# Kernel optimization log

Measured on AMD Instinct MI355X. Metric: run time of the kernel, lower is better.

The kernel has to match this reference:

```python
import jax, jax.numpy as jnp
import numpy as np

# Static config (matches init_kwargs)
B, S = 4, 1024            # prefill: 4 sequences of 1024 tokens (num_tokens = 4096)
H = 16                    # num_heads
NOPE, ROPE, VD = 128, 64, 128
RANK = 512                # kv_lora_rank
SCALE = 0.07216878364870323  # 1/sqrt(head_dim=192)


def setup_inputs() -> dict:
    key = jax.random.key(0)
    k1, k2, k3, k4 = jax.random.split(key, 4)
    T = B * S
    return {
        "q": jax.random.normal(k1, (T, H, NOPE + ROPE), dtype=jnp.float32),
        "compressed_kv": jax.random.normal(k2, (T, RANK), dtype=jnp.float32),
        "rope_k": jax.random.normal(k3, (T, ROPE), dtype=jnp.float32),
        "w_up": jax.random.normal(k4, (H * (NOPE + VD), RANK), dtype=jnp.float32) * 0.02,
    }


def reference(q, compressed_kv, rope_k, w_up):
    T = q.shape[0]
    # Up-project latent -> per-head (k_nope, v): [T, H, NOPE+VD]
    kv = (compressed_kv @ w_up.T).reshape(B, S, H, NOPE + VD)
    k_nope = kv[..., :NOPE]          # [B,S,H,NOPE]
    v = kv[..., NOPE:]               # [B,S,H,VD]

    qb = q.reshape(B, S, H, NOPE + ROPE)
    q_nope = qb[..., :NOPE]          # [B,S,H,NOPE]
    q_rope = qb[..., NOPE:]          # [B,S,H,ROPE]
    rk = rope_k.reshape(B, S, ROPE)  # head-shared RoPE K component

    # Attention logits: nope part (per-head K) + rope part (shared K)
    scores = jnp.einsum('bqhd,bkhd->bhqk', q_nope, k_nope)
    scores = scores + jnp.einsum('bqhd,bkd->bhqk', q_rope, rk)
    scores = scores * SCALE

    # Causal mask within each sequence
    causal = jnp.tril(jnp.ones((S, S), dtype=bool))
    scores = jnp.where(causal[None, None], scores, jnp.finfo(scores.dtype).min)

    p = jax.nn.softmax(scores, axis=-1)                 # [B,H,S,S]
    out = jnp.einsum('bhqk,bkhd->bqhd', p, v)           # [B,S,H,VD]
    return out.reshape(T, H, VD)
```

## Files before the change

### kernel.cpp

```cpp
#include <hip/hip_runtime.h>
#include <stdint.h>


#define Hz 16
#define Sz 1024
#define RANKz 512
#define SCALEf 0.07216878364870323f
#define CRr(r) ((((r) & 3)) + 8 * ((r) >> 2) + 4 * hi)

typedef unsigned short u16;
typedef __attribute__((ext_vector_type(8))) short bf16x8;
typedef __attribute__((ext_vector_type(4))) float f32x4;
typedef __attribute__((ext_vector_type(16))) float f32x16;

__device__ __forceinline__ u16 f2b(float f) {
  union { float f; uint32_t u; } x; x.f = f;
  return (u16)((x.u + 0x7fffu + ((x.u >> 16) & 1u)) >> 16);
}
__device__ __forceinline__ uint32_t cvtpk(float lo, float hi_) {
  uint32_t r;
  asm("v_cvt_pk_bf16_f32 %0, %1, %2" : "=v"(r) : "v"(lo), "v"(hi_));
  return r;
}

__global__ void cvt_bf16_kernel(const float* __restrict__ a, u16* __restrict__ ao,
                                const float* __restrict__ b, u16* __restrict__ bo,
                                const float* __restrict__ c, u16* __restrict__ co,
                                int na, int nb) {
  int idx = blockIdx.x * blockDim.x + threadIdx.x;
  const float* s; u16* d; int i;
  if (idx < na)            { s = a; d = ao; i = idx; }
  else if (idx < na + nb)  { s = b; d = bo; i = idx - na; }
  else                     { s = c; d = co; i = idx - na - nb; }
  float4 v = ((const float4*)s)[i];
  ushort4 o = make_ushort4(f2b(v.x), f2b(v.y), f2b(v.z), f2b(v.w));
  ((ushort4*)d)[i] = o;
}

__global__ __launch_bounds__(256)
void gemm_kv_bf16(const u16* __restrict__ A,
                  const u16* __restrict__ Bm,
                  u16* __restrict__ C) {
  __shared__ u16 As[128 * 32];
  __shared__ u16 Bs[128 * 32];
  const int tid = threadIdx.x;
  const int w = tid >> 6, lane = tid & 63;
  const int wr = w >> 1, wc = w & 1;
  const int row0 = blockIdx.x * 128, col0 = blockIdx.y * 128;
  f32x4 acc[4][4];
#pragma unroll
  for (int m = 0; m < 4; ++m)
#pragma unroll
    for (int n = 0; n < 4; ++n) acc[m][n] = (f32x4){0.f, 0.f, 0.f, 0.f};

  const int rstage = (lane >> 2);
  const int cstage = (lane & 3) * 8;

  for (int kt = 0; kt < RANKz / 32; ++kt) {
    const int k0 = kt * 32;
#pragma unroll
    for (int i = 0; i < 2; ++i) {
      const int chunk = i * 4 + w;
      const int r = chunk * 16 + rstage;
      const u16* ga = A  + (size_t)(row0 + r) * RANKz + k0 + cstage;
      const u16* gb = Bm + (size_t)(col0 + r) * RANKz + k0 + cstage;
      __builtin_amdgcn_global_load_lds((const __attribute__((address_space(1))) void*)ga,
                                       (__attribute__((address_space(3))) void*)&As[chunk * 512], 16, 0, 0);
      __builtin_amdgcn_global_load_lds((const __attribute__((address_space(1))) void*)gb,
                                       (__attribute__((address_space(3))) void*)&Bs[chunk * 512], 16, 0, 0);
    }
    __syncthreads();
    const int klo = (lane >> 4) * 8;
    bf16x8 af[4], bfr[4];
#pragma unroll
    for (int m = 0; m < 4; ++m)
      af[m] = *(const bf16x8*)&As[(wr * 64 + m * 16 + (lane & 15)) * 32 + klo];
#pragma unroll
    for (int n = 0; n < 4; ++n)
      bfr[n] = *(const bf16x8*)&Bs[(wc * 64 + n * 16 + (lane & 15)) * 32 + klo];
#pragma unroll
    for (int m = 0; m < 4; ++m)
#pragma unroll
      for (int n = 0; n < 4; ++n)
        acc[m][n] = __builtin_amdgcn_mfma_f32_16x16x32_bf16(af[m], bfr[n], acc[m][n], 0, 0, 0);
    __syncthreads();
  }
  const int cb = col0 + wc * 64 + (lane & 15);
  const int rb = row0 + wr * 64 + (lane >> 4) * 4;
#pragma unroll
  for (int m = 0; m < 4; ++m)
#pragma unroll
    for (int n = 0; n < 4; ++n)
#pragma unroll
      for (int j = 0; j < 4; ++j)
        C[(size_t)(rb + m * 16 + j) * 4096 + (cb + n * 16)] = f2b(acc[m][n][j]);
}

__global__ __launch_bounds__(512, 2)
void mla_attn_mfma(const float* __restrict__ q,
                   const u16* __restrict__ kvb,
                   const u16* __restrict__ ropeb,
                   float* __restrict__ out) {
  __shared__ __align__(16) unsigned char LB[81920];

  const int tid = threadIdx.x;
  const int w = tid >> 6, lane = tid & 63;
  const int l31 = lane & 31, hi = lane >> 5;
  const int half = w >> 2, strip = w & 3;

  const int bid = blockIdx.x;
  const int hb = bid >> 6;
  const int qt = (hb < 4) ? (7 - hb) : (hb - 4);
  const int bh = (bid & 7) * 8 + ((bid >> 3) & 7);
  const int bat = bh >> 4, h = bh & 15;
  const int tok0 = bat * Sz;
  const int q0 = qt * 128 + strip * 32;
  const int ntiles = 2 * qt + 2;

  const int vkp = tid & 31, vdc = tid >> 5;
  uint4 va, vb;

  auto stageK = [&](int tokt, int buf) {
#pragma unroll
    for (int i = 0; i < 2; ++i) {
      const int c = w * 2 + i;
      const int row = c * 4 + (lane >> 4);
      const int sc = (lane & 15) ^ (row & 7);
      const u16* src = kvb + ((size_t)(tokt + row) * Hz + h) * 256 + sc * 8;
      __builtin_amdgcn_global_load_lds((const __attribute__((address_space(1))) void*)src,
                                       (__attribute__((address_space(3))) void*)(LB + buf * 16384 + c * 1024), 16, 0, 0);
    }
    {
      const int c = w;
      const int row = c * 8 + (lane >> 3);
      const int sc = (lane & 7) ^ (row & 7);
      const u16* src = ropeb + (size_t)(tokt + row) * 64 + sc * 8;
      __builtin_amdgcn_global_load_lds((const __attribute__((address_space(1))) void*)src,
                                       (__attribute__((address_space(3))) void*)(LB + 32768 + buf * 8192 + c * 1024), 16, 0, 0);
    }
  };
  auto loadV = [&](int tokt) {
    const u16* vp = kvb + ((size_t)(tokt + vkp * 2) * Hz + h) * 256 + 128 + vdc * 8;
    va = *(const uint4*)vp;
    vb = *(const uint4*)(vp + Hz * 256);
  };
  auto writeVt = [&](int buf) {
    union { uint4 v; u16 u[8]; } A_, B_;
    A_.v = va; B_.v = vb;
    uint32_t* vt = (uint32_t*)(LB + 49152 + buf * 16384);
#pragma unroll
    for (int i = 0; i < 8; ++i) {
      const int d = vdc * 8 + i;
      vt[d * 32 + 4 * ((vkp >> 2) ^ (d & 7)) + (vkp & 3)] =
          (uint32_t)A_.u[i] | ((uint32_t)B_.u[i] << 16);
    }
  };

  bf16x8 qf[12];
  {
    const float* qp = q + ((size_t)(tok0 + q0 + l31) * Hz + h) * 192 + hi * 8;
#pragma unroll
    for (int ds = 0; ds < 12; ++ds) {
      float4 a = *(const float4*)(qp + ds * 16);
      float4 b = *(const float4*)(qp + ds * 16 + 4);
      union { bf16x8 v; u16 u[8]; } t;
      t.u[0] = f2b(a.x * SCALEf); t.u[1] = f2b(a.y * SCALEf);
      t.u[2] = f2b(a.z * SCALEf); t.u[3] = f2b(a.w * SCALEf);
      t.u[4] = f2b(b.x * SCALEf); t.u[5] = f2b(b.y * SCALEf);
      t.u[6] = f2b(b.z * SCALEf); t.u[7] = f2b(b.w * SCALEf);
      qf[ds] = t.v;
    }
  }

  f32x16 acc[4];
#pragma unroll
  for (int db = 0; db < 4; ++db)
#pragma unroll
    for (int r = 0; r < 16; ++r) acc[db][r] = 0.f;
  float m_run = -1e30f, l_run = 0.f;

  stageK(tok0, 0);
  loadV(tok0);
  __syncthreads();
  writeVt(0);
  __syncthreads();

#pragma unroll 1
  for (int t = 0; t < ntiles; ++t) {
    const int cur = t & 1;
    const bool havenext = (t + 1 < ntiles);
    if (havenext) {
      stageK(tok0 + (t + 1) * 64, cur ^ 1);
      loadV(tok0 + (t + 1) * 64);
    }

    const int kb = t * 64 + half * 32;
    if (kb <= q0 + 31) {
      const u16* KnC = (const u16*)(LB + cur * 16384);
      const u16* KrC = (const u16*)(LB + 32768 + cur * 8192);
      const int row_a = half * 32 + l31;
      const int swz = row_a & 7;

      f32x16 s0;
#pragma unroll
      for (int r = 0; r < 16; ++r) s0[r] = 0.f;
      __builtin_amdgcn_s_setprio(1);
#pragma unroll
      for (int ds = 0; ds < 8; ++ds) {
        bf16x8 kf = *(const bf16x8*)&KnC[row_a * 128 + 8 * ((2 * ds + hi) ^ swz)];
        s0 = __builtin_amdgcn_mfma_f32_32x32x16_bf16(kf, qf[ds], s0, 0, 0, 0);
      }
#pragma unroll
      for (int ds = 8; ds < 12; ++ds) {
        bf16x8 kf = *(const bf16x8*)&KrC[row_a * 64 + 8 * ((2 * (ds - 8) + hi) ^ swz)];
        s0 = __builtin_amdgcn_mfma_f32_32x32x16_bf16(kf, qf[ds], s0, 0, 0, 0);
      }
      __builtin_amdgcn_s_setprio(0);

      if (kb + 31 > q0) {
#pragma unroll
        for (int r = 0; r < 16; ++r)
          if (kb + CRr(r) > q0 + l31) s0[r] = -1e30f;
      }

      float mx = s0[0];
#pragma unroll
      for (int r = 1; r < 16; ++r) mx = fmaxf(mx, s0[r]);
      mx = fmaxf(mx, __shfl_xor(mx, 32));
      if (__any(mx > m_run + 8.f)) {
        const float nm = fmaxf(m_run, mx);
        const float cr = __expf(m_run - nm);
        m_run = nm; l_run *= cr;
#pragma unroll
        for (int r = 0; r < 16; ++r) {
          const float crg = __shfl(cr, CRr(r));
#pragma unroll
          for (int db = 0; db < 4; ++db) acc[db][r] *= crg;
        }
      }
      float ts = 0.f;
#pragma unroll
      for (int r = 0; r < 16; ++r) { s0[r] = __expf(s0[r] - m_run); ts += s0[r]; }
      ts += __shfl_xor(ts, 32);
      l_run += ts;

      bf16x8 pf[2];
#pragma unroll
      for (int ks = 0; ks < 2; ++ks) {
        const int o = ks * 8;
        const uint32_t w0 = cvtpk(s0[o + 0], s0[o + 1]);
        const uint32_t w1 = cvtpk(s0[o + 4], s0[o + 5]);
        const uint32_t w2 = cvtpk(s0[o + 2], s0[o + 3]);
        const uint32_t w3 = cvtpk(s0[o + 6], s0[o + 7]);
        const uint32_t t0 = __shfl_xor(w0, 32), t1 = __shfl_xor(w1, 32);
        const uint32_t t2 = __shfl_xor(w2, 32), t3 = __shfl_xor(w3, 32);
        union { bf16x8 v; uint32_t u[4]; } P;
        P.u[0] = hi ? t1 : w0;
        P.u[1] = hi ? t3 : w2;
        P.u[2] = hi ? w1 : t0;
        P.u[3] = hi ? w3 : t2;
        pf[ks] = P.v;
      }

      const u16* VtC = (const u16*)(LB + 49152 + cur * 16384);
      __builtin_amdgcn_s_setprio(1);
#pragma unroll
      for (int ks = 0; ks < 2; ++ks)
#pragma unroll
        for (int db = 0; db < 4; ++db) {
          const int d = db * 32 + l31;
          bf16x8 vf = *(const bf16x8*)&VtC[d * 64 + 8 * ((half * 4 + 2 * ks + hi) ^ (d & 7))];
          acc[db] = __builtin_amdgcn_mfma_f32_32x32x16_bf16(pf[ks], vf, acc[db], 0, 0, 0);
        }
      __builtin_amdgcn_s_setprio(0);
    }

    if (havenext) writeVt(cur ^ 1);
    __syncthreads();
  }

  float* mb = (float*)LB;
  float* ml = (float*)(LB + 65536);
  if (half == 1) {
#pragma unroll
    for (int db = 0; db < 4; ++db)
#pragma unroll
      for (int g = 0; g < 4; ++g) {
        float4 v = make_float4(acc[db][g * 4 + 0], acc[db][g * 4 + 1],
                               acc[db][g * 4 + 2], acc[db][g * 4 + 3]);
        *(float4*)&mb[strip * 4096 + db * 1024 + g * 256 + lane * 4] = v;
      }
    if (lane < 32) { ml[strip * 64 + lane] = m_run; ml[strip * 64 + 32 + lane] = l_run; }
  }
  __syncthreads();
  if (half == 0) {
    const float mp = ml[strip * 64 + l31];
    const float lp = ml[strip * 64 + 32 + l31];
    const float M  = fmaxf(m_run, mp);
    const float sA = __expf(m_run - M);
    const float sB = __expf(mp - M);
    const float inv = 1.0f / (l_run * sA + lp * sB);
    const float fAl = sA * inv, fBl = sB * inv;
    float fA[16], fB[16];
#pragma unroll
    for (int r = 0; r < 16; ++r) { fA[r] = __shfl(fAl, CRr(r)); fB[r] = __shfl(fBl, CRr(r)); }
#pragma unroll
    for (int db = 0; db < 4; ++db)
#pragma unroll
      for (int g = 0; g < 4; ++g) {
        float4 pv = *(const float4*)&mb[strip * 4096 + db * 1024 + g * 256 + lane * 4];
#pragma unroll
        for (int jj = 0; jj < 4; ++jj) {
          const int r = g * 4 + jj;
          const float pvj = (jj == 0) ? pv.x : (jj == 1) ? pv.y : (jj == 2) ? pv.z : pv.w;
          out[((size_t)(tok0 + q0 + CRr(r)) * Hz + h) * 128 + db * 32 + l31] =
              acc[db][r] * fA[r] + pvj * fB[r];
        }
      }
  }
}

extern "C" void kernel_launch(void* const* d_in, const int* in_sizes, int n_in,
                              void* d_out, int out_size, void* d_ws, size_t ws_size,
                              hipStream_t stream) {
  const float* q    = (const float*)d_in[0];
  const float* ckv  = (const float*)d_in[1];
  const float* rope = (const float*)d_in[2];
  const float* wup  = (const float*)d_in[3];
  float* out = (float*)d_out;

  u16* ckvb  = (u16*)d_ws;
  u16* wupb  = ckvb + (size_t)4096 * RANKz;
  u16* kvb   = wupb + (size_t)4096 * RANKz;
  u16* ropeb = kvb + (size_t)4096 * 4096;

  const int nvec = 4096 * RANKz / 4;
  const int nrope = 4096 * 64 / 4;
  cvt_bf16_kernel<<<(2 * nvec + nrope) / 256, 256, 0, stream>>>(ckv, ckvb, wup, wupb, rope, ropeb, nvec, nvec);

  dim3 gg(32, 32);
  gemm_kv_bf16<<<gg, 256, 0, stream>>>(ckvb, wupb, kvb);

  mla_attn_mfma<<<512, 512, 0, stream>>>(q, kvb, ropeb, out);
}
```

Measured before the change: 105.3 us.

## Pair causal q-tiles per block and triple-buffer K/V with distance-2 prefetch

Each block now processes two query tiles (qt and 7-qt) in sequence, so every block does the same amount of causal work. The grid halves to 256 blocks at one block per CU. K, rope-K and V tiles are triple-buffered with prefetch two tiles ahead, using explicit vmcnt waits and raw barriers in place of __syncthreads. LDS grows to about 121KB and occupancy drops to one block per CU, which risks less latency hiding between blocks. The max and sum reductions are also rewritten as trees.

```diff
diff --git a/kernel.cpp b/kernel.cpp
--- a/kernel.cpp
+++ b/kernel.cpp
@@ -96,12 +96,12 @@
         C[(size_t)(rb + m * 16 + j) * 4096 + (cb + n * 16)] = f2b(acc[m][n][j]);
 }
 
-__global__ __launch_bounds__(512, 2)
+__global__ __launch_bounds__(512, 1)
 void mla_attn_mfma(const float* __restrict__ q,
                    const u16* __restrict__ kvb,
                    const u16* __restrict__ ropeb,
                    float* __restrict__ out) {
-  __shared__ __align__(16) unsigned char LB[81920];
+  __shared__ __align__(16) unsigned char LB[123904];
 
   const int tid = threadIdx.x;
   const int w = tid >> 6, lane = tid & 63;
@@ -109,16 +109,12 @@
   const int half = w >> 2, strip = w & 3;
 
   const int bid = blockIdx.x;
-  const int hb = bid >> 6;
-  const int qt = (hb < 4) ? (7 - hb) : (hb - 4);
-  const int bh = (bid & 7) * 8 + ((bid >> 3) & 7);
+  const int job = (bid & 7) * 32 + (bid >> 3);
+  const int bh = job >> 2, pr = job & 3;
   const int bat = bh >> 4, h = bh & 15;
   const int tok0 = bat * Sz;
-  const int q0 = qt * 128 + strip * 32;
-  const int ntiles = 2 * qt + 2;
 
   const int vkp = tid & 31, vdc = tid >> 5;
-  uint4 va, vb;
 
   auto stageK = [&](int tokt, int buf) {
 #pragma unroll
@@ -136,18 +132,18 @@
       const int sc = (lane & 7) ^ (row & 7);
       const u16* src = ropeb + (size_t)(tokt + row) * 64 + sc * 8;
       __builtin_amdgcn_global_load_lds((const __attribute__((address_space(1))) void*)src,
-                                       (__attribute__((address_space(3))) void*)(LB + 32768 + buf * 8192 + c * 1024), 16, 0, 0);
+                                       (__attribute__((address_space(3))) void*)(LB + 49152 + buf * 8192 + c * 1024), 16, 0, 0);
     }
   };
-  auto loadV = [&](int tokt) {
+  auto loadV = [&](int tokt, uint4& va, uint4& vb) {
     const u16* vp = kvb + ((size_t)(tokt + vkp * 2) * Hz + h) * 256 + 128 + vdc * 8;
     va = *(const uint4*)vp;
     vb = *(const uint4*)(vp + Hz * 256);
   };
-  auto writeVt = [&](int buf) {
+  auto writeVt = [&](int buf, uint4 va, uint4 vb) {
     union { uint4 v; u16 u[8]; } A_, B_;
     A_.v = va; B_.v = vb;
-    uint32_t* vt = (uint32_t*)(LB + 49152 + buf * 16384);
+    uint32_t* vt = (uint32_t*)(LB + 73728 + buf * 16384);
 #pragma unroll
     for (int i = 0; i < 8; ++i) {
       const int d = vdc * 8 + i;
@@ -156,167 +152,194 @@
     }
   };
 
-  bf16x8 qf[12];
-  {
-    const float* qp = q + ((size_t)(tok0 + q0 + l31) * Hz + h) * 192 + hi * 8;
-#pragma unroll
-    for (int ds = 0; ds < 12; ++ds) {
-      float4 a = *(const float4*)(qp + ds * 16);
-      float4 b = *(const float4*)(qp + ds * 16 + 4);
-      union { bf16x8 v; u16 u[8]; } t;
-      t.u[0] = f2b(a.x * SCALEf); t.u[1] = f2b(a.y * SCALEf);
-      t.u[2] = f2b(a.z * SCALEf); t.u[3] = f2b(a.w * SCALEf);
-      t.u[4] = f2b(b.x * SCALEf); t.u[5] = f2b(b.y * SCALEf);
-      t.u[6] = f2b(b.z * SCALEf); t.u[7] = f2b(b.w * SCALEf);
-      qf[ds] = t.v;
-    }
-  }
-
-  f32x16 acc[4];
-#pragma unroll
-  for (int db = 0; db < 4; ++db)
-#pragma unroll
-    for (int r = 0; r < 16; ++r) acc[db][r] = 0.f;
-  float m_run = -1e30f, l_run = 0.f;
-
-  stageK(tok0, 0);
-  loadV(tok0);
-  __syncthreads();
-  writeVt(0);
-  __syncthreads();
-
 #pragma unroll 1
-  for (int t = 0; t < ntiles; ++t) {
-    const int cur = t & 1;
-    const bool havenext = (t + 1 < ntiles);
-    if (havenext) {
-      stageK(tok0 + (t + 1) * 64, cur ^ 1);
-      loadV(tok0 + (t + 1) * 64);
-    }
-
-    const int kb = t * 64 + half * 32;
-    if (kb <= q0 + 31) {
-      const u16* KnC = (const u16*)(LB + cur * 16384);
-      const u16* KrC = (const u16*)(LB + 32768 + cur * 8192);
-      const int row_a = half * 32 + l31;
-      const int swz = row_a & 7;
-
-      f32x16 s0;
-#pragma unroll
-      for (int r = 0; r < 16; ++r) s0[r] = 0.f;
-      __builtin_amdgcn_s_setprio(1);
-#pragma unroll
-      for (int ds = 0; ds < 8; ++ds) {
-        bf16x8 kf = *(const bf16x8*)&KnC[row_a * 128 + 8 * ((2 * ds + hi) ^ swz)];
-        s0 = __builtin_amdgcn_mfma_f32_32x32x16_bf16(kf, qf[ds], s0, 0, 0, 0);
+  for (int pass = 0; pass < 2; ++pass) {
+    const int qt = pass ? pr : (7 - pr);
+    const int nt = 2 * qt + 2;
+    const int q0 = qt * 128 + strip * 32;
+
+    bf16x8 qf[12];
+    {
+      const float* qp = q + ((size_t)(tok0 + q0 + l31) * Hz + h) * 192 + hi * 8;
+#pragma unroll
+      for (int ds = 0; ds < 12; ++ds) {
+        float4 a = *(const float4*)(qp + ds * 16);
+        float4 b = *(const float4*)(qp + ds * 16 + 4);
+        union { bf16x8 v; u16 u[8]; } t;
+        t.u[0] = f2b(a.x * SCALEf); t.u[1] = f2b(a.y * SCALEf);
+        t.u[2] = f2b(a.z * SCALEf); t.u[3] = f2b(a.w * SCALEf);
+        t.u[4] = f2b(b.x * SCALEf); t.u[5] = f2b(b.y * SCALEf);
+        t.u[6] = f2b(b.z * SCALEf); t.u[7] = f2b(b.w * SCALEf);
+        qf[ds] = t.v;
       }
-#pragma unroll
-      for (int ds = 8; ds < 12; ++ds) {
-        bf16x8 kf = *(const bf16x8*)&KrC[row_a * 64 + 8 * ((2 * (ds - 8) + hi) ^ swz)];
-        s0 = __builtin_amdgcn_mfma_f32_32x32x16_bf16(kf, qf[ds], s0, 0, 0, 0);
+    }
+
+    f32x16 acc[4];
+#pragma unroll
+    for (int db = 0; db < 4; ++db)
+#pragma unroll
+      for (int r = 0; r < 16; ++r) acc[db][r] = 0.f;
+    float m_run = -1e30f, l_run = 0.f;
+
+    uint4 vaA, vbA, vaB, vbB;
+
+    stageK(tok0, 0);            loadV(tok0, vaA, vbA);
+    stageK(tok0 + 64, 1);       loadV(tok0 + 64, vaB, vbB);
+    writeVt(0, vaA, vbA);
+    asm volatile("s_waitcnt vmcnt(5) lgkmcnt(0)" ::: "memory");
+    __builtin_amdgcn_s_barrier();
+    __builtin_amdgcn_sched_barrier(0);
+
+    auto round = [&](int t, uint4& iva, uint4& ivb, uint4& wva, uint4& wvb) {
+      const bool issue = (t + 2 < nt);
+      if (issue) {
+        stageK(tok0 + (t + 2) * 64, (t + 2) % 3);
+        loadV(tok0 + (t + 2) * 64, iva, ivb);
       }
-      __builtin_amdgcn_s_setprio(0);
-
-      if (kb + 31 > q0) {
-#pragma unroll
-        for (int r = 0; r < 16; ++r)
-          if (kb + CRr(r) > q0 + l31) s0[r] = -1e30f;
+
+      const int kb = t * 64 + half * 32;
+      if (kb <= q0 + 31) {
+        const int bufC = t % 3;
+        const u16* KnC = (const u16*)(LB + bufC * 16384);
+        const u16* KrC = (const u16*)(LB + 49152 + bufC * 8192);
+        const u16* VtC = (const u16*)(LB + 73728 + bufC * 16384);
+        const int row_a = half * 32 + l31;
+        const int swz = row_a & 7;
+
+        f32x16 s0;
+#pragma unroll
+        for (int r = 0; r < 16; ++r) s0[r] = 0.f;
+        __builtin_amdgcn_s_setprio(1);
+#pragma unroll
+        for (int ds = 0; ds < 8; ++ds) {
+          bf16x8 kf = *(const bf16x8*)&KnC[row_a * 128 + 8 * ((2 * ds + hi) ^ swz)];
+          s0 = __builtin_amdgcn_mfma_f32_32x32x16_bf16(kf, qf[ds], s0, 0, 0, 0);
+        }
+#pragma unroll
+        for (int ds = 0; ds < 4; ++ds) {
+          bf16x8 kf = *(const bf16x8*)&KrC[row_a * 64 + 8 * ((2 * ds + hi) ^ swz)];
+          s0 = __builtin_amdgcn_mfma_f32_32x32x16_bf16(kf, qf[8 + ds], s0, 0, 0, 0);
+        }
+        __builtin_amdgcn_s_setprio(0);
+
+        if (kb + 31 > q0) {
+#pragma unroll
+          for (int r = 0; r < 16; ++r)
+            if (kb + CRr(r) > q0 + l31) s0[r] = -1e30f;
+        }
+
+        float ma0 = fmaxf(s0[0], s0[1]),   ma1 = fmaxf(s0[2], s0[3]);
+        float ma2 = fmaxf(s0[4], s0[5]),   ma3 = fmaxf(s0[6], s0[7]);
+        float ma4 = fmaxf(s0[8], s0[9]),   ma5 = fmaxf(s0[10], s0[11]);
+        float ma6 = fmaxf(s0[12], s0[13]), ma7 = fmaxf(s0[14], s0[15]);
+        float mx = fmaxf(fmaxf(fmaxf(ma0, ma1), fmaxf(ma2, ma3)),
+                         fmaxf(fmaxf(ma4, ma5), fmaxf(ma6, ma7)));
+        mx = fmaxf(mx, __shfl_xor(mx, 32));
+        if (__any(mx > m_run + 8.f)) {
+          const float nm = fmaxf(m_run, mx);
+          const float cr = __expf(m_run - nm);
+          m_run = nm; l_run *= cr;
+#pragma unroll
+          for (int r = 0; r < 16; ++r) {
+            const float crg = __shfl(cr, CRr(r));
+#pragma unroll
+            for (int db = 0; db < 4; ++db) acc[db][r] *= crg;
+          }
+        }
+#pragma unroll
+        for (int r = 0; r < 16; ++r) s0[r] = __expf(s0[r] - m_run);
+        float e0 = s0[0] + s0[1],   e1 = s0[2] + s0[3];
+        float e2 = s0[4] + s0[5],   e3 = s0[6] + s0[7];
+        float e4 = s0[8] + s0[9],   e5 = s0[10] + s0[11];
+        float e6 = s0[12] + s0[13], e7 = s0[14] + s0[15];
+        float ts = ((e0 + e1) + (e2 + e3)) + ((e4 + e5) + (e6 + e7));
+        ts += __shfl_xor(ts, 32);
+        l_run += ts;
+
+        bf16x8 pf[2];
+#pragma unroll
+        for (int ks = 0; ks < 2; ++ks) {
+          const int o = ks * 8;
+          const uint32_t w0 = cvtpk(s0[o + 0], s0[o + 1]);
+          const uint32_t w1 = cvtpk(s0[o + 4], s0[o + 5]);
+          const uint32_t w2 = cvtpk(s0[o + 2], s0[o + 3]);
+          const uint32_t w3 = cvtpk(s0[o + 6], s0[o + 7]);
+          const uint32_t t0 = __shfl_xor(w0, 32), t1 = __shfl_xor(w1, 32);
+          const uint32_t t2 = __shfl_xor(w2, 32), t3 = __shfl_xor(w3, 32);
+          union { bf16x8 v; uint32_t u[4]; } P;
+          P.u[0] = hi ? t1 : w0;
+          P.u[1] = hi ? t3 : w2;
+          P.u[2] = hi ? w1 : t0;
+          P.u[3] = hi ? w3 : t2;
+          pf[ks] = P.v;
+        }
+
+        __builtin_amdgcn_s_setprio(1);
+#pragma unroll
+        for (int ks = 0; ks < 2; ++ks)
+#pragma unroll
+          for (int db = 0; db < 4; ++db) {
+            const int d = db * 32 + l31;
+            bf16x8 vf = *(const bf16x8*)&VtC[d * 64 + 8 * ((half * 4 + 2 * ks + hi) ^ (d & 7))];
+            acc[db] = __builtin_amdgcn_mfma_f32_32x32x16_bf16(pf[ks], vf, acc[db], 0, 0, 0);
+          }
+        __builtin_amdgcn_s_setprio(0);
       }
 
-      float mx = s0[0];
-#pragma unroll
-      for (int r = 1; r < 16; ++r) mx = fmaxf(mx, s0[r]);
-      mx = fmaxf(mx, __shfl_xor(mx, 32));
-      if (__any(mx > m_run + 8.f)) {
-        const float nm = fmaxf(m_run, mx);
-        const float cr = __expf(m_run - nm);
-        m_run = nm; l_run *= cr;
-#pragma unroll
-        for (int r = 0; r < 16; ++r) {
-          const float crg = __shfl(cr, CRr(r));
-#pragma unroll
-          for (int db = 0; db < 4; ++db) acc[db][r] *= crg;
-        }
-      }
-      float ts = 0.f;
-#pragma unroll
-      for (int r = 0; r < 16; ++r) { s0[r] = __expf(s0[r] - m_run); ts += s0[r]; }
-      ts += __shfl_xor(ts, 32);
-      l_run += ts;
-
-      bf16x8 pf[2];
-#pragma unroll
-      for (int ks = 0; ks < 2; ++ks) {
-        const int o = ks * 8;
-        const uint32_t w0 = cvtpk(s0[o + 0], s0[o + 1]);
-        const uint32_t w1 = cvtpk(s0[o + 4], s0[o + 5]);
-        const uint32_t w2 = cvtpk(s0[o + 2], s0[o + 3]);
-        const uint32_t w3 = cvtpk(s0[o + 6], s0[o + 7]);
-        const uint32_t t0 = __shfl_xor(w0, 32), t1 = __shfl_xor(w1, 32);
-        const uint32_t t2 = __shfl_xor(w2, 32), t3 = __shfl_xor(w3, 32);
-        union { bf16x8 v; uint32_t u[4]; } P;
-        P.u[0] = hi ? t1 : w0;
-        P.u[1] = hi ? t3 : w2;
-        P.u[2] = hi ? w1 : t0;
-        P.u[3] = hi ? w3 : t2;
-        pf[ks] = P.v;
-      }
-
-      const u16* VtC = (const u16*)(LB + 49152 + cur * 16384);
-      __builtin_amdgcn_s_setprio(1);
-#pragma unroll
-      for (int ks = 0; ks < 2; ++ks)
-#pragma unroll
-        for (int db = 0; db < 4; ++db) {
-          const int d = db * 32 + l31;
-          bf16x8 vf = *(const bf16x8*)&VtC[d * 64 + 8 * ((half * 4 + 2 * ks + hi) ^ (d & 7))];
-          acc[db] = __builtin_amdgcn_mfma_f32_32x32x16_bf16(pf[ks], vf, acc[db], 0, 0, 0);
-        }
-      __builtin_amdgcn_s_setprio(0);
-    }
-
-    if (havenext) writeVt(cur ^ 1);
+      if (t + 1 < nt) writeVt((t + 1) % 3, wva, wvb);
+
+      if (issue) { asm volatile("s_waitcnt vmcnt(5) lgkmcnt(0)" ::: "memory"); }
+      else       { asm volatile("s_waitcnt vmcnt(0) lgkmcnt(0)" ::: "memory"); }
+      __builtin_amdgcn_s_barrier();
+      __builtin_amdgcn_sched_barrier(0);
+    };
+
+#pragma unroll 1
+    for (int t = 0; t < nt; t += 2) {
+      round(t,     vaA, vbA, vaB, vbB);
+      round(t + 1, vaB, vbB, vaA, vbA);
+    }
+
+    float* mb = (float*)LB;
+    float* ml = (float*)(LB + 122880);
+    if (half == 1) {
+#pragma unroll
+      for (int db = 0; db < 4; ++db)
+#pragma unroll
+        for (int g = 0; g < 4; ++g) {
+          float4 v = make_float4(acc[db][g * 4 + 0], acc[db][g * 4 + 1],
+                                 acc[db][g * 4 + 2], acc[db][g * 4 + 3]);
+          *(float4*)&mb[strip * 4096 + db * 1024 + g * 256 + lane * 4] = v;
+        }
+      if (lane < 32) { ml[strip * 64 + lane] = m_run; ml[strip * 64 + 32 + lane] = l_run; }
+    }
     __syncthreads();
-  }
-
-  float* mb = (float*)LB;
-  float* ml = (float*)(LB + 65536);
-  if (half == 1) {
-#pragma unroll
-    for (int db = 0; db < 4; ++db)
-#pragma unroll
-      for (int g = 0; g < 4; ++g) {
-        float4 v = make_float4(acc[db][g * 4 + 0], acc[db][g * 4 + 1],
-                               acc[db][g * 4 + 2], acc[db][g * 4 + 3]);
-        *(float4*)&mb[strip * 4096 + db * 1024 + g * 256 + lane * 4] = v;
-      }
-    if (lane < 32) { ml[strip * 64 + lane] = m_run; ml[strip * 64 + 32 + lane] = l_run; }
-  }
-  __syncthreads();
-  if (half == 0) {
-    const float mp = ml[strip * 64 + l31];
-    const float lp = ml[strip * 64 + 32 + l31];
-    const float M  = fmaxf(m_run, mp);
-    const float sA = __expf(m_run - M);
-    const float sB = __expf(mp - M);
-    const float inv = 1.0f / (l_run * sA + lp * sB);
-    const float fAl = sA * inv, fBl = sB * inv;
-    float fA[16], fB[16];
-#pragma unroll
-    for (int r = 0; r < 16; ++r) { fA[r] = __shfl(fAl, CRr(r)); fB[r] = __shfl(fBl, CRr(r)); }
-#pragma unroll
-    for (int db = 0; db < 4; ++db)
-#pragma unroll
-      for (int g = 0; g < 4; ++g) {
-        float4 pv = *(const float4*)&mb[strip * 4096 + db * 1024 + g * 256 + lane * 4];
-#pragma unroll
-        for (int jj = 0; jj < 4; ++jj) {
-          const int r = g * 4 + jj;
-          const float pvj = (jj == 0) ? pv.x : (jj == 1) ? pv.y : (jj == 2) ? pv.z : pv.w;
-          out[((size_t)(tok0 + q0 + CRr(r)) * Hz + h) * 128 + db * 32 + l31] =
-              acc[db][r] * fA[r] + pvj * fB[r];
-        }
-      }
+    if (half == 0) {
+      const float mp = ml[strip * 64 + l31];
+      const float lp = ml[strip * 64 + 32 + l31];
+      const float M  = fmaxf(m_run, mp);
+      const float sA = __expf(m_run - M);
+      const float sB = __expf(mp - M);
+      const float inv = 1.0f / (l_run * sA + lp * sB);
+      const float fAl = sA * inv, fBl = sB * inv;
+      float fA[16], fB[16];
+#pragma unroll
+      for (int r = 0; r < 16; ++r) { fA[r] = __shfl(fAl, CRr(r)); fB[r] = __shfl(fBl, CRr(r)); }
+#pragma unroll
+      for (int db = 0; db < 4; ++db)
+#pragma unroll
+        for (int g = 0; g < 4; ++g) {
+          float4 pv = *(const float4*)&mb[strip * 4096 + db * 1024 + g * 256 + lane * 4];
+#pragma unroll
+          for (int jj = 0; jj < 4; ++jj) {
+            const int r = g * 4 + jj;
+            const float pvj = (jj == 0) ? pv.x : (jj == 1) ? pv.y : (jj == 2) ? pv.z : pv.w;
+            out[((size_t)(tok0 + q0 + CRr(r)) * Hz + h) * 128 + db * 32 + l31] =
+                acc[db][r] * fA[r] + pvj * fB[r];
+          }
+        }
+    }
+    __syncthreads();
   }
 }
 
@@ -341,5 +364,5 @@
   dim3 gg(32, 32);
   gemm_kv_bf16<<<gg, 256, 0, stream>>>(ckvb, wupb, kvb);
 
-  mla_attn_mfma<<<512, 512, 0, stream>>>(q, kvb, ropeb, out);
-}
+  mla_attn_mfma<<<256, 512, 0, stream>>>(q, kvb, ropeb, out);
+}
```

Result: faster. 102.9 us (-2.3%).
